# Kernel tuning notes

Measured on AMD Instinct MI355X. Metric: run time of the kernel, lower is better.

Reference implementation:

```python
import jax, jax.numpy as jnp
import numpy as np

EMB = 768
HEADS = 8
HEAD_DIM = EMB // HEADS
SCALE = HEAD_DIM ** -0.5


def setup_inputs() -> dict:
    key = jax.random.key(0)
    ks = jax.random.split(key, 9)
    s = EMB ** -0.5
    return {
        "x": jax.random.normal(ks[0], (2, 4096, EMB), dtype=jnp.float32),
        "Wq": jax.random.normal(ks[1], (EMB, EMB), dtype=jnp.float32) * s,
        "bq": jax.random.normal(ks[2], (EMB,), dtype=jnp.float32) * 0.02,
        "Wk": jax.random.normal(ks[3], (EMB, EMB), dtype=jnp.float32) * s,
        "bk": jax.random.normal(ks[4], (EMB,), dtype=jnp.float32) * 0.02,
        "Wv": jax.random.normal(ks[5], (EMB, EMB), dtype=jnp.float32) * s,
        "bv": jax.random.normal(ks[6], (EMB,), dtype=jnp.float32) * 0.02,
        "Wo": jax.random.normal(ks[7], (EMB, EMB), dtype=jnp.float32) * s,
        "bo": jax.random.normal(ks[8], (EMB,), dtype=jnp.float32) * 0.02,
    }


def reference(x, Wq, bq, Wk, bk, Wv, bv, Wo, bo):
    b, n, _ = x.shape
    def split_heads(t):  # [b, n, emb] -> [b, h, n, d]
        return t.reshape(b, n, HEADS, HEAD_DIM).transpose(0, 2, 1, 3)
    q = split_heads(x @ Wq + bq)
    k = split_heads(x @ Wk + bk)
    v = split_heads(x @ Wv + bv)
    scores = jnp.einsum('bhqd,bhkd->bhqk', q, k)
    # NOTE: faithful to source — softmax first, THEN multiply by scale.
    attn = jax.nn.softmax(scores, axis=-1) * SCALE
    out = jnp.einsum('bhqk,bhkd->bhqd', attn, v)
    out = out.transpose(0, 2, 1, 3).reshape(b, n, EMB)
    return out @ Wo + bo
```

## Files before the change

### kernel.cpp

```cpp
#include <hip/hip_runtime.h>
#include <hip/hip_fp16.h>


typedef _Float16 half8 __attribute__((ext_vector_type(8)));
typedef _Float16 half4 __attribute__((ext_vector_type(4)));
typedef float   float4_ __attribute__((ext_vector_type(4)));
typedef float   f32x16 __attribute__((ext_vector_type(16)));

#define EMB   768
#define NSEQ  4096
#define MTOT  8192
#define SCALE 0.102062072615966f

__device__ __forceinline__ float4_ mfma16(half8 a, half8 b, float4_ c) {
    return __builtin_amdgcn_mfma_f32_16x16x32_f16(a, b, c, 0, 0, 0);
}
__device__ __forceinline__ f32x16 mfma32(half8 a, half8 b, f32x16 c) {
    return __builtin_amdgcn_mfma_f32_32x32x16_f16(a, b, c, 0, 0, 0);
}


__global__ void cast_x(const float* __restrict__ x, _Float16* __restrict__ xb) {
    int i = blockIdx.x * 256 + threadIdx.x;
    float4_ v = ((const float4_*)x)[i];
    half4 h = { (_Float16)v[0], (_Float16)v[1], (_Float16)v[2], (_Float16)v[3] };
    ((half4*)xb)[i] = h;
}

__global__ void prep_w(const float* __restrict__ Wq, const float* __restrict__ Wk,
                       const float* __restrict__ Wv, const float* __restrict__ Wo,
                       _Float16* __restrict__ wqkv, _Float16* __restrict__ wot) {
    int k = blockIdx.x * 256 + threadIdx.x;
    int r = blockIdx.y;
    if (r < 2304) {
        const float* W = (r < 768) ? Wq : (r < 1536) ? Wk : Wv;
        int c = r % 768;
        wqkv[(size_t)r * 768 + k] = (_Float16)W[(size_t)k * 768 + c];
    } else {
        int c = r - 2304;
        wot[(size_t)c * 768 + k] = (_Float16)Wo[(size_t)k * 768 + c];
    }
}

__global__ void prep_bias(const float* __restrict__ bq, const float* __restrict__ bk,
                          const float* __restrict__ bv, float* __restrict__ bqkv) {
    int i = blockIdx.x * 256 + threadIdx.x;
    float v = (i < 768) ? bq[i] : (i < 1536) ? bk[i - 768] : bv[i - 1536];
    bqkv[i] = v;
}

__global__ __launch_bounds__(256, 2) void gemm_kernel(
    const _Float16* __restrict__ A, const _Float16* __restrict__ Bt,
    const float* __restrict__ bias, int mode,
    _Float16* __restrict__ Qo, _Float16* __restrict__ Ko, _Float16* __restrict__ Vto,
    float* __restrict__ out)
{
    __shared__ alignas(16) _Float16 Al[128 * 72];
    __shared__ alignas(16) _Float16 Bl[64 * 72];
    const int tid = threadIdx.x;
    const int lane = tid & 63, w = tid >> 6;
    const int wm = w >> 1, wn = w & 1;
    const int l15 = lane & 15, l4 = lane >> 4;
    const int m0 = blockIdx.y * 128;
    const int n0 = blockIdx.x * 64;

    float4_ acc[4][2] = {};

    for (int k0 = 0; k0 < 768; k0 += 64) {
        #pragma unroll
        for (int it = 0; it < 4; ++it) {
            int idx = it * 256 + tid;
            int row = idx >> 3, c8 = idx & 7;
            *(half8*)(Al + row * 72 + c8 * 8) =
                *(const half8*)(A + (size_t)(m0 + row) * 768 + k0 + c8 * 8);
        }
        #pragma unroll
        for (int it = 0; it < 2; ++it) {
            int idx = it * 256 + tid;
            int row = idx >> 3, c8 = idx & 7;
            *(half8*)(Bl + row * 72 + c8 * 8) =
                *(const half8*)(Bt + (size_t)(n0 + row) * 768 + k0 + c8 * 8);
        }
        __syncthreads();
        #pragma unroll
        for (int kc = 0; kc < 2; ++kc) {
            half8 bfr[2];
            #pragma unroll
            for (int nt = 0; nt < 2; ++nt)
                bfr[nt] = *(const half8*)(Bl + (wn * 32 + nt * 16 + l15) * 72 + kc * 32 + 8 * l4);
            #pragma unroll
            for (int mt = 0; mt < 4; ++mt) {
                half8 afr = *(const half8*)(Al + (wm * 64 + mt * 16 + l15) * 72 + kc * 32 + 8 * l4);
                #pragma unroll
                for (int nt = 0; nt < 2; ++nt)
                    acc[mt][nt] = mfma16(afr, bfr[nt], acc[mt][nt]);
            }
        }
        __syncthreads();
    }

    #pragma unroll
    for (int mt = 0; mt < 4; ++mt)
    #pragma unroll
    for (int nt = 0; nt < 2; ++nt) {
        int gc = n0 + wn * 32 + nt * 16 + l15;
        float bv_ = bias[gc];
        #pragma unroll
        for (int r = 0; r < 4; ++r) {
            int gm = m0 + wm * 64 + mt * 16 + l4 * 4 + r;
            float val = acc[mt][nt][r] + bv_;
            if (mode == 1) {
                out[(size_t)gm * 768 + gc] = val;
            } else {
                int b = gm >> 12, n = gm & 4095;
                _Float16 hv = (_Float16)val;
                if (gc < 768) {
                    int h = gc / 96, d = gc % 96;
                    Qo[(((size_t)(b * 8 + h)) * 4096 + n) * 96 + d] = hv;
                } else if (gc < 1536) {
                    int c = gc - 768, h = c / 96, d = c % 96;
                    int bh = b * 8 + h;
                    size_t idx = (((size_t)bh * 128 + (n >> 5)) * 6 + (d >> 4)) * 512
                               + (size_t)((d >> 3) & 1) * 256 + (size_t)(n & 31) * 8 + (d & 7);
                    Ko[idx] = hv;
                } else {
                    int c = gc - 1536, h = c / 96, d = c % 96;
                    int bh = b * 8 + h;
                    size_t idx = (((size_t)bh * 64 + (n >> 6)) * 12 + ((n >> 4) & 3) * 3 + (d >> 5)) * 512
                               + (size_t)((n >> 3) & 1) * 256 + (size_t)(d & 31) * 8 + (n & 7);
                    Vto[idx] = hv;
                }
            }
        }
    }
}

__global__ __launch_bounds__(256, 2) void attn_kernel(
    const _Float16* __restrict__ Q, const _Float16* __restrict__ Kf,
    const _Float16* __restrict__ Vf, _Float16* __restrict__ AO)
{
    __shared__ alignas(16) _Float16 lds[2][24 * 512];
    __shared__ float tab[4][32];

    const int tid = threadIdx.x;
    const int lane = tid & 63, w = tid >> 6;
    const int l31 = lane & 31, hi = lane >> 5;

    const int B = blockIdx.x;
    const int xcd = B & 7, j = B >> 3;
    const int bh = 2 * xcd + (j >> 5);
    const int qb = j & 31;
    const int q0 = qb * 128 + w * 32;

    const size_t qBase = (size_t)bh * 4096 * 96;
    const _Float16* kfb = Kf + (size_t)bh * 393216;
    const _Float16* vfb = Vf + (size_t)bh * 393216;

    half8 qf[6];
    #pragma unroll
    for (int dch = 0; dch < 6; ++dch)
        qf[dch] = *(const half8*)(Q + qBase + (size_t)(q0 + l31) * 96 + dch * 16 + hi * 8);

    f32x16 o0 = {}, o1 = {}, o2 = {};
    float m_run = -1e30f, l_run = 0.f;

    const int fbase = w * 6;
    half8 streg[6];

    #pragma unroll
    for (int i = 0; i < 6; ++i) {
        int f = fbase + i;
        const _Float16* g = (f < 12 ? kfb + (size_t)f * 512
                                    : vfb + (size_t)(f - 12) * 512) + lane * 8;
        streg[i] = *(const half8*)g;
    }
    #pragma unroll
    for (int i = 0; i < 6; ++i)
        *(half8*)(&lds[0][(fbase + i) * 512 + lane * 8]) = streg[i];
    __syncthreads();

    int cur = 0;
    for (int t = 0; t < 64; ++t) {
        const int tn = (t + 1) & 63;
        #pragma unroll
        for (int i = 0; i < 6; ++i) {
            int f = fbase + i;
            const _Float16* g = (f < 12 ? kfb + ((size_t)tn * 12 + f) * 512
                                        : vfb + ((size_t)tn * 12 + (f - 12)) * 512) + lane * 8;
            streg[i] = *(const half8*)g;
        }

        const _Float16* kb = &lds[cur][0];
        const _Float16* vb = &lds[cur][12 * 512];

        f32x16 s0 = {}, s1 = {};
        __builtin_amdgcn_s_setprio(1);
        #pragma unroll
        for (int dch = 0; dch < 6; ++dch) {
            half8 k0 = *(const half8*)(kb + (0 * 6 + dch) * 512 + lane * 8);
            half8 k1 = *(const half8*)(kb + (1 * 6 + dch) * 512 + lane * 8);
            s0 = mfma32(k0, qf[dch], s0);
            s1 = mfma32(k1, qf[dch], s1);
        }
        __builtin_amdgcn_s_setprio(0);

        float lm = s0[0];
        #pragma unroll
        for (int r = 1; r < 16; ++r) lm = fmaxf(lm, s0[r]);
        #pragma unroll
        for (int r = 0; r < 16; ++r) lm = fmaxf(lm, s1[r]);
        float pmax = fmaxf(lm, __shfl_xor(lm, 32));
        if (__any(pmax > m_run + 4.0f)) {
            float mnew = fmaxf(m_run, pmax);
            float al = __expf(m_run - mnew);
            m_run = mnew;
            l_run *= al;
            if (hi == 0) tab[w][l31] = al;
            asm volatile("s_waitcnt lgkmcnt(0)" ::: "memory");
            #pragma unroll
            for (int r = 0; r < 16; ++r) {
                float alr = tab[w][(r & 3) + 8 * (r >> 2) + 4 * hi];
                o0[r] *= alr; o1[r] *= alr; o2[r] *= alr;
            }
        }
        float ls = 0.f;
        uint32_t Lp0[8], Lp1[8];
        #pragma unroll
        for (int jg = 0; jg < 4; ++jg) {
            float p0 = __expf(s0[4 * jg + 0] - m_run);
            float p1 = __expf(s0[4 * jg + 1] - m_run);
            float p2 = __expf(s0[4 * jg + 2] - m_run);
            float p3 = __expf(s0[4 * jg + 3] - m_run);
            ls += (p0 + p1) + (p2 + p3);
            union { _Float16 h[2]; uint32_t u; } a, b2;
            a.h[0] = (_Float16)p0; a.h[1] = (_Float16)p1;
            b2.h[0] = (_Float16)p2; b2.h[1] = (_Float16)p3;
            Lp0[jg * 2] = a.u; Lp0[jg * 2 + 1] = b2.u;
        }
        #pragma unroll
        for (int jg = 0; jg < 4; ++jg) {
            float p0 = __expf(s1[4 * jg + 0] - m_run);
            float p1 = __expf(s1[4 * jg + 1] - m_run);
            float p2 = __expf(s1[4 * jg + 2] - m_run);
            float p3 = __expf(s1[4 * jg + 3] - m_run);
            ls += (p0 + p1) + (p2 + p3);
            union { _Float16 h[2]; uint32_t u; } a, b2;
            a.h[0] = (_Float16)p0; a.h[1] = (_Float16)p1;
            b2.h[0] = (_Float16)p2; b2.h[1] = (_Float16)p3;
            Lp1[jg * 2] = a.u; Lp1[jg * 2 + 1] = b2.u;
        }
        l_run += ls + __shfl_xor(ls, 32);

        half8 pa[4];
        #pragma unroll
        for (int kc = 0; kc < 2; ++kc) {
            uint32_t a0 = Lp0[4 * kc], a1 = Lp0[4 * kc + 1];
            uint32_t a2 = Lp0[4 * kc + 2], a3 = Lp0[4 * kc + 3];
            uint32_t w0 = __shfl_xor((int)a0, 32), w1 = __shfl_xor((int)a1, 32);
            uint32_t w2 = __shfl_xor((int)a2, 32), w3 = __shfl_xor((int)a3, 32);
            union { half8 h; uint32_t u[4]; } fr;
            fr.u[0] = hi ? w2 : a0;  fr.u[1] = hi ? w3 : a1;
            fr.u[2] = hi ? a2 : w0;  fr.u[3] = hi ? a3 : w1;
            pa[kc] = fr.h;
        }
        #pragma unroll
        for (int kc = 0; kc < 2; ++kc) {
            uint32_t a0 = Lp1[4 * kc], a1 = Lp1[4 * kc + 1];
            uint32_t a2 = Lp1[4 * kc + 2], a3 = Lp1[4 * kc + 3];
            uint32_t w0 = __shfl_xor((int)a0, 32), w1 = __shfl_xor((int)a1, 32);
            uint32_t w2 = __shfl_xor((int)a2, 32), w3 = __shfl_xor((int)a3, 32);
            union { half8 h; uint32_t u[4]; } fr;
            fr.u[0] = hi ? w2 : a0;  fr.u[1] = hi ? w3 : a1;
            fr.u[2] = hi ? a2 : w0;  fr.u[3] = hi ? a3 : w1;
            pa[2 + kc] = fr.h;
        }

        __builtin_amdgcn_s_setprio(1);
        #pragma unroll
        for (int kk = 0; kk < 4; ++kk) {
            half8 v0 = *(const half8*)(vb + (kk * 3 + 0) * 512 + lane * 8);
            half8 v1 = *(const half8*)(vb + (kk * 3 + 1) * 512 + lane * 8);
            half8 v2 = *(const half8*)(vb + (kk * 3 + 2) * 512 + lane * 8);
            o0 = mfma32(pa[kk], v0, o0);
            o1 = mfma32(pa[kk], v1, o1);
            o2 = mfma32(pa[kk], v2, o2);
        }
        __builtin_amdgcn_s_setprio(0);

        __syncthreads();
        #pragma unroll
        for (int i = 0; i < 6; ++i)
            *(half8*)(&lds[cur ^ 1][(fbase + i) * 512 + lane * 8]) = streg[i];
        __syncthreads();
        cur ^= 1;
    }

    if (hi == 0) tab[w][l31] = l_run;
    asm volatile("s_waitcnt lgkmcnt(0)" ::: "memory");
    const int b = bh >> 3, h = bh & 7;
    #pragma unroll
    for (int r = 0; r < 16; ++r) {
        int qrow = (r & 3) + 8 * (r >> 2) + 4 * hi;
        float inv = SCALE / tab[w][qrow];
        int n = q0 + qrow;
        size_t base = ((size_t)(b * 4096 + n)) * 768 + h * 96 + l31;
        AO[base]      = (_Float16)(o0[r] * inv);
        AO[base + 32] = (_Float16)(o1[r] * inv);
        AO[base + 64] = (_Float16)(o2[r] * inv);
    }
}


extern "C" void kernel_launch(void* const* d_in, const int* in_sizes, int n_in,
                              void* d_out, int out_size, void* d_ws, size_t ws_size,
                              hipStream_t stream) {
    const float* x  = (const float*)d_in[0];
    const float* Wq = (const float*)d_in[1];
    const float* bq = (const float*)d_in[2];
    const float* Wk = (const float*)d_in[3];
    const float* bk = (const float*)d_in[4];
    const float* Wv = (const float*)d_in[5];
    const float* bv = (const float*)d_in[6];
    const float* Wo = (const float*)d_in[7];
    const float* bo = (const float*)d_in[8];
    float* out = (float*)d_out;

    char* ws = (char*)d_ws;
    _Float16* xb   = (_Float16*)(ws);
    _Float16* wqkv = (_Float16*)(ws + 12582912);
    _Float16* wot  = (_Float16*)(ws + 16121856);
    float*    bqkv = (float*)   (ws + 17301504);
    _Float16* Qb   = (_Float16*)(ws + 17310720);
    _Float16* Kfb  = (_Float16*)(ws + 29893632);
    _Float16* Vfb  = (_Float16*)(ws + 42476544);
    _Float16* AO   = xb;

    cast_x<<<6144, 256, 0, stream>>>(x, xb);
    prep_w<<<dim3(3, 3072), 256, 0, stream>>>(Wq, Wk, Wv, Wo, wqkv, wot);
    prep_bias<<<9, 256, 0, stream>>>(bq, bk, bv, bqkv);

    gemm_kernel<<<dim3(36, 64), 256, 0, stream>>>(xb, wqkv, bqkv, 0, Qb, Kfb, Vfb, nullptr);

    attn_kernel<<<512, 256, 0, stream>>>(Qb, Kfb, Vfb, AO);

    gemm_kernel<<<dim3(12, 64), 256, 0, stream>>>(AO, wot, bo, 1, nullptr, nullptr, nullptr, out);
}
```

Measured before the change: 281.5 us.

## Tile transpose in prep_w, direct-to-LDS loads, bigger GEMM tiles, two query groups per attention wave

The weight prep now transposes through a shared-memory tile with vectorized, coalesced reads and writes. The GEMM switches to 128x128 tiles loaded straight into LDS with global_load_lds, stored in fragment order. The attention kernel processes 64 query rows per wave as two groups, so each K/V LDS load feeds twice the MFMA work. The attention kernel also fetches the next K/V tile directly into LDS, drops one barrier, folds log2e into Q for exp2, raises the rescale threshold, and uses permlane32_swap instead of shuffles. The cost is higher register pressure (launch bounds of 1) and half as many attention blocks (256 instead of 512), which may underfill the GPU.

```diff
diff --git a/kernel.cpp b/kernel.cpp
--- a/kernel.cpp
+++ b/kernel.cpp
@@ -7,16 +7,19 @@
 typedef float   float4_ __attribute__((ext_vector_type(4)));
 typedef float   f32x16 __attribute__((ext_vector_type(16)));
 
-#define EMB   768
-#define NSEQ  4096
-#define MTOT  8192
 #define SCALE 0.102062072615966f
+#define LOG2E 1.44269504088896340736f
 
 __device__ __forceinline__ float4_ mfma16(half8 a, half8 b, float4_ c) {
     return __builtin_amdgcn_mfma_f32_16x16x32_f16(a, b, c, 0, 0, 0);
 }
 __device__ __forceinline__ f32x16 mfma32(half8 a, half8 b, f32x16 c) {
     return __builtin_amdgcn_mfma_f32_32x32x16_f16(a, b, c, 0, 0, 0);
+}
+__device__ __forceinline__ void gload16(const _Float16* g, _Float16* l) {
+    __builtin_amdgcn_global_load_lds(
+        (const __attribute__((address_space(1))) void*)g,
+        (__attribute__((address_space(3))) void*)l, 16, 0, 0);
 }
 
 
@@ -30,16 +33,34 @@
 __global__ void prep_w(const float* __restrict__ Wq, const float* __restrict__ Wk,
                        const float* __restrict__ Wv, const float* __restrict__ Wo,
                        _Float16* __restrict__ wqkv, _Float16* __restrict__ wot) {
-    int k = blockIdx.x * 256 + threadIdx.x;
-    int r = blockIdx.y;
-    if (r < 2304) {
-        const float* W = (r < 768) ? Wq : (r < 1536) ? Wk : Wv;
-        int c = r % 768;
-        wqkv[(size_t)r * 768 + k] = (_Float16)W[(size_t)k * 768 + c];
-    } else {
-        int c = r - 2304;
-        wot[(size_t)c * 768 + k] = (_Float16)Wo[(size_t)k * 768 + c];
-    }
+    __shared__ float tile[64][65];
+    const int bid = blockIdx.x;
+    const int mat = bid / 144, rem = bid % 144;
+    const int kt = rem / 12, ct = rem % 12;
+    const float* W = (mat == 0) ? Wq : (mat == 1) ? Wk : (mat == 2) ? Wv : Wo;
+    const int k0 = kt * 64, c0 = ct * 64;
+    const int t = threadIdx.x;
+    const int lr = t >> 4, lc = (t & 15) * 4;
+    #pragma unroll
+    for (int i = 0; i < 4; ++i) {
+        float4_ v = *(const float4_*)(W + (size_t)(k0 + i * 16 + lr) * 768 + c0 + lc);
+        tile[i * 16 + lr][lc + 0] = v[0];
+        tile[i * 16 + lr][lc + 1] = v[1];
+        tile[i * 16 + lr][lc + 2] = v[2];
+        tile[i * 16 + lr][lc + 3] = v[3];
+    }
+    __syncthreads();
+    const int cr = t >> 2, kq = (t & 3) * 16;
+    _Float16* dst = (mat < 3) ? (wqkv + ((size_t)(mat * 768 + c0 + cr)) * 768 + k0 + kq)
+                              : (wot  + ((size_t)(c0 + cr)) * 768 + k0 + kq);
+    half8 h0, h1;
+    #pragma unroll
+    for (int j = 0; j < 8; ++j) {
+        h0[j] = (_Float16)tile[kq + j][cr];
+        h1[j] = (_Float16)tile[kq + 8 + j][cr];
+    }
+    *(half8*)dst = h0;
+    *(half8*)(dst + 8) = h1;
 }
 
 __global__ void prep_bias(const float* __restrict__ bq, const float* __restrict__ bk,
@@ -55,44 +76,44 @@
     _Float16* __restrict__ Qo, _Float16* __restrict__ Ko, _Float16* __restrict__ Vto,
     float* __restrict__ out)
 {
-    __shared__ alignas(16) _Float16 Al[128 * 72];
-    __shared__ alignas(16) _Float16 Bl[64 * 72];
+    __shared__ alignas(16) _Float16 Af[16 * 512];
+    __shared__ alignas(16) _Float16 Bf[16 * 512];
     const int tid = threadIdx.x;
     const int lane = tid & 63, w = tid >> 6;
     const int wm = w >> 1, wn = w & 1;
     const int l15 = lane & 15, l4 = lane >> 4;
     const int m0 = blockIdx.y * 128;
-    const int n0 = blockIdx.x * 64;
-
-    float4_ acc[4][2] = {};
+    const int n0 = blockIdx.x * 128;
+
+    const _Float16* gs[8];
+    _Float16* ld[8];
+    #pragma unroll
+    for (int i = 0; i < 8; ++i) {
+        int f = (w & 1) * 8 + i;
+        int rg = f >> 1, kc = f & 1;
+        int r0 = ((w < 2) ? m0 : n0) + rg * 16;
+        gs[i] = ((w < 2) ? A : Bt) + (size_t)(r0 + l15) * 768 + kc * 32 + l4 * 8;
+        ld[i] = ((w < 2) ? Af : Bf) + f * 512;
+    }
+
+    float4_ acc[4][4] = {};
 
     for (int k0 = 0; k0 < 768; k0 += 64) {
         #pragma unroll
-        for (int it = 0; it < 4; ++it) {
-            int idx = it * 256 + tid;
-            int row = idx >> 3, c8 = idx & 7;
-            *(half8*)(Al + row * 72 + c8 * 8) =
-                *(const half8*)(A + (size_t)(m0 + row) * 768 + k0 + c8 * 8);
-        }
-        #pragma unroll
-        for (int it = 0; it < 2; ++it) {
-            int idx = it * 256 + tid;
-            int row = idx >> 3, c8 = idx & 7;
-            *(half8*)(Bl + row * 72 + c8 * 8) =
-                *(const half8*)(Bt + (size_t)(n0 + row) * 768 + k0 + c8 * 8);
-        }
+        for (int i = 0; i < 8; ++i)
+            gload16(gs[i] + k0, ld[i]);
         __syncthreads();
         #pragma unroll
         for (int kc = 0; kc < 2; ++kc) {
-            half8 bfr[2];
+            half8 bfr[4];
             #pragma unroll
-            for (int nt = 0; nt < 2; ++nt)
-                bfr[nt] = *(const half8*)(Bl + (wn * 32 + nt * 16 + l15) * 72 + kc * 32 + 8 * l4);
+            for (int nt = 0; nt < 4; ++nt)
+                bfr[nt] = *(const half8*)(Bf + (size_t)(((wn * 4 + nt) * 2 + kc) * 512 + lane * 8));
             #pragma unroll
             for (int mt = 0; mt < 4; ++mt) {
-                half8 afr = *(const half8*)(Al + (wm * 64 + mt * 16 + l15) * 72 + kc * 32 + 8 * l4);
+                half8 afr = *(const half8*)(Af + (size_t)(((wm * 4 + mt) * 2 + kc) * 512 + lane * 8));
                 #pragma unroll
-                for (int nt = 0; nt < 2; ++nt)
+                for (int nt = 0; nt < 4; ++nt)
                     acc[mt][nt] = mfma16(afr, bfr[nt], acc[mt][nt]);
             }
         }
@@ -102,8 +123,8 @@
     #pragma unroll
     for (int mt = 0; mt < 4; ++mt)
     #pragma unroll
-    for (int nt = 0; nt < 2; ++nt) {
-        int gc = n0 + wn * 32 + nt * 16 + l15;
+    for (int nt = 0; nt < 4; ++nt) {
+        int gc = n0 + wn * 64 + nt * 16 + l15;
         float bv_ = bias[gc];
         #pragma unroll
         for (int r = 0; r < 4; ++r) {
@@ -113,34 +134,33 @@
                 out[(size_t)gm * 768 + gc] = val;
             } else {
                 int b = gm >> 12, n = gm & 4095;
-                _Float16 hv = (_Float16)val;
                 if (gc < 768) {
                     int h = gc / 96, d = gc % 96;
-                    Qo[(((size_t)(b * 8 + h)) * 4096 + n) * 96 + d] = hv;
+                    Qo[(((size_t)(b * 8 + h)) * 4096 + n) * 96 + d] = (_Float16)(val * LOG2E);
                 } else if (gc < 1536) {
                     int c = gc - 768, h = c / 96, d = c % 96;
                     int bh = b * 8 + h;
                     size_t idx = (((size_t)bh * 128 + (n >> 5)) * 6 + (d >> 4)) * 512
                                + (size_t)((d >> 3) & 1) * 256 + (size_t)(n & 31) * 8 + (d & 7);
-                    Ko[idx] = hv;
+                    Ko[idx] = (_Float16)val;
                 } else {
                     int c = gc - 1536, h = c / 96, d = c % 96;
                     int bh = b * 8 + h;
                     size_t idx = (((size_t)bh * 64 + (n >> 6)) * 12 + ((n >> 4) & 3) * 3 + (d >> 5)) * 512
                                + (size_t)((n >> 3) & 1) * 256 + (size_t)(d & 31) * 8 + (n & 7);
-                    Vto[idx] = hv;
+                    Vto[idx] = (_Float16)val;
                 }
             }
         }
     }
 }
 
-__global__ __launch_bounds__(256, 2) void attn_kernel(
+__global__ __launch_bounds__(256, 1) void attn_kernel(
     const _Float16* __restrict__ Q, const _Float16* __restrict__ Kf,
     const _Float16* __restrict__ Vf, _Float16* __restrict__ AO)
 {
-    __shared__ alignas(16) _Float16 lds[2][24 * 512];
-    __shared__ float tab[4][32];
+    __shared__ alignas(16) _Float16 kvbuf[2][24 * 512];
+    __shared__ float tab[4][64];
 
     const int tid = threadIdx.x;
     const int lane = tid & 63, w = tid >> 6;
@@ -148,132 +168,114 @@
 
     const int B = blockIdx.x;
     const int xcd = B & 7, j = B >> 3;
-    const int bh = 2 * xcd + (j >> 5);
-    const int qb = j & 31;
-    const int q0 = qb * 128 + w * 32;
+    const int bh = 2 * xcd + (j >> 4);
+    const int qb = j & 15;
+    const int q0 = qb * 256 + w * 64;
 
     const size_t qBase = (size_t)bh * 4096 * 96;
     const _Float16* kfb = Kf + (size_t)bh * 393216;
     const _Float16* vfb = Vf + (size_t)bh * 393216;
 
-    half8 qf[6];
-    #pragma unroll
-    for (int dch = 0; dch < 6; ++dch)
-        qf[dch] = *(const half8*)(Q + qBase + (size_t)(q0 + l31) * 96 + dch * 16 + hi * 8);
-
-    f32x16 o0 = {}, o1 = {}, o2 = {};
-    float m_run = -1e30f, l_run = 0.f;
+    half8 qf[2][6];
+    #pragma unroll
+    for (int g = 0; g < 2; ++g)
+        #pragma unroll
+        for (int dch = 0; dch < 6; ++dch)
+            qf[g][dch] = *(const half8*)(Q + qBase + (size_t)(q0 + g * 32 + l31) * 96 + dch * 16 + hi * 8);
+
+    f32x16 oA0 = {}, oA1 = {}, oA2 = {}, oB0 = {}, oB1 = {}, oB2 = {};
+    float mA = -1e30f, lA = 0.f, mB = -1e30f, lB = 0.f;
 
     const int fbase = w * 6;
-    half8 streg[6];
-
+    const _Float16* gsrc[6];
     #pragma unroll
     for (int i = 0; i < 6; ++i) {
         int f = fbase + i;
-        const _Float16* g = (f < 12 ? kfb + (size_t)f * 512
-                                    : vfb + (size_t)(f - 12) * 512) + lane * 8;
-        streg[i] = *(const half8*)g;
-    }
+        gsrc[i] = ((f < 12) ? (kfb + (size_t)f * 512) : (vfb + (size_t)(f - 12) * 512)) + lane * 8;
+    }
+
     #pragma unroll
     for (int i = 0; i < 6; ++i)
-        *(half8*)(&lds[0][(fbase + i) * 512 + lane * 8]) = streg[i];
+        gload16(gsrc[i], &kvbuf[0][(fbase + i) * 512]);
     __syncthreads();
+
+    auto softmax_group = [&](f32x16& s0, f32x16& s1, float& m, float& l,
+                             f32x16& o0, f32x16& o1, f32x16& o2, int trow, half8* pa) {
+        float lm = fmaxf(s0[0], s0[1]);
+        #pragma unroll
+        for (int r = 2; r < 16; ++r) lm = fmaxf(lm, s0[r]);
+        #pragma unroll
+        for (int r = 0; r < 16; ++r) lm = fmaxf(lm, s1[r]);
+        float pmax = fmaxf(lm, __shfl_xor(lm, 32));
+        if (__any(pmax > m + 8.0f)) {
+            float mn = fmaxf(m, pmax);
+            float al = __builtin_exp2f(m - mn);
+            m = mn; l *= al;
+            if (hi == 0) tab[w][trow + l31] = al;
+            asm volatile("s_waitcnt lgkmcnt(0)" ::: "memory");
+            #pragma unroll
+            for (int r = 0; r < 16; ++r) {
+                float alr = tab[w][trow + (r & 3) + 8 * (r >> 2) + 4 * hi];
+                o0[r] *= alr; o1[r] *= alr; o2[r] *= alr;
+            }
+        }
+        float ls = 0.f;
+        uint32_t Lp[16];
+        #pragma unroll
+        for (int kg = 0; kg < 2; ++kg) {
+            const f32x16& s = kg ? s1 : s0;
+            #pragma unroll
+            for (int jg = 0; jg < 4; ++jg) {
+                float p0 = __builtin_exp2f(s[4 * jg + 0] - m);
+                float p1 = __builtin_exp2f(s[4 * jg + 1] - m);
+                float p2 = __builtin_exp2f(s[4 * jg + 2] - m);
+                float p3 = __builtin_exp2f(s[4 * jg + 3] - m);
+                ls += (p0 + p1) + (p2 + p3);
+                union { _Float16 h[2]; uint32_t u; } pk0, pk1;
+                pk0.h[0] = (_Float16)p0; pk0.h[1] = (_Float16)p1;
+                pk1.h[0] = (_Float16)p2; pk1.h[1] = (_Float16)p3;
+                Lp[kg * 8 + jg * 2] = pk0.u; Lp[kg * 8 + jg * 2 + 1] = pk1.u;
+            }
+        }
+        l += ls + __shfl_xor(ls, 32);
+        #pragma unroll
+        for (int kk = 0; kk < 4; ++kk) {
+            uint32_t u0 = Lp[4 * kk], u1 = Lp[4 * kk + 1];
+            uint32_t u2 = Lp[4 * kk + 2], u3 = Lp[4 * kk + 3];
+            asm("v_permlane32_swap_b32 %0, %1" : "+v"(u0), "+v"(u2));
+            asm("v_permlane32_swap_b32 %0, %1" : "+v"(u1), "+v"(u3));
+            union { half8 h; uint32_t u[4]; } fr;
+            fr.u[0] = u0; fr.u[1] = u1; fr.u[2] = u2; fr.u[3] = u3;
+            pa[kk] = fr.h;
+        }
+    };
 
     int cur = 0;
     for (int t = 0; t < 64; ++t) {
         const int tn = (t + 1) & 63;
         #pragma unroll
-        for (int i = 0; i < 6; ++i) {
-            int f = fbase + i;
-            const _Float16* g = (f < 12 ? kfb + ((size_t)tn * 12 + f) * 512
-                                        : vfb + ((size_t)tn * 12 + (f - 12)) * 512) + lane * 8;
-            streg[i] = *(const half8*)g;
-        }
-
-        const _Float16* kb = &lds[cur][0];
-        const _Float16* vb = &lds[cur][12 * 512];
-
-        f32x16 s0 = {}, s1 = {};
+        for (int i = 0; i < 6; ++i)
+            gload16(gsrc[i] + (size_t)tn * 6144, &kvbuf[cur ^ 1][(fbase + i) * 512]);
+
+        const _Float16* kb = &kvbuf[cur][0];
+        const _Float16* vb = &kvbuf[cur][12 * 512];
+
+        f32x16 sA0 = {}, sA1 = {}, sB0 = {}, sB1 = {};
         __builtin_amdgcn_s_setprio(1);
         #pragma unroll
         for (int dch = 0; dch < 6; ++dch) {
-            half8 k0 = *(const half8*)(kb + (0 * 6 + dch) * 512 + lane * 8);
-            half8 k1 = *(const half8*)(kb + (1 * 6 + dch) * 512 + lane * 8);
-            s0 = mfma32(k0, qf[dch], s0);
-            s1 = mfma32(k1, qf[dch], s1);
+            half8 k0 = *(const half8*)(kb + (dch) * 512 + lane * 8);
+            half8 k1 = *(const half8*)(kb + (6 + dch) * 512 + lane * 8);
+            sA0 = mfma32(k0, qf[0][dch], sA0);
+            sB0 = mfma32(k0, qf[1][dch], sB0);
+            sA1 = mfma32(k1, qf[0][dch], sA1);
+            sB1 = mfma32(k1, qf[1][dch], sB1);
         }
         __builtin_amdgcn_s_setprio(0);
 
-        float lm = s0[0];
-        #pragma unroll
-        for (int r = 1; r < 16; ++r) lm = fmaxf(lm, s0[r]);
-        #pragma unroll
-        for (int r = 0; r < 16; ++r) lm = fmaxf(lm, s1[r]);
-        float pmax = fmaxf(lm, __shfl_xor(lm, 32));
-        if (__any(pmax > m_run + 4.0f)) {
-            float mnew = fmaxf(m_run, pmax);
-            float al = __expf(m_run - mnew);
-            m_run = mnew;
-            l_run *= al;
-            if (hi == 0) tab[w][l31] = al;
-            asm volatile("s_waitcnt lgkmcnt(0)" ::: "memory");
-            #pragma unroll
-            for (int r = 0; r < 16; ++r) {
-                float alr = tab[w][(r & 3) + 8 * (r >> 2) + 4 * hi];
-                o0[r] *= alr; o1[r] *= alr; o2[r] *= alr;
-            }
-        }
-        float ls = 0.f;
-        uint32_t Lp0[8], Lp1[8];
-        #pragma unroll
-        for (int jg = 0; jg < 4; ++jg) {
-            float p0 = __expf(s0[4 * jg + 0] - m_run);
-            float p1 = __expf(s0[4 * jg + 1] - m_run);
-            float p2 = __expf(s0[4 * jg + 2] - m_run);
-            float p3 = __expf(s0[4 * jg + 3] - m_run);
-            ls += (p0 + p1) + (p2 + p3);
-            union { _Float16 h[2]; uint32_t u; } a, b2;
-            a.h[0] = (_Float16)p0; a.h[1] = (_Float16)p1;
-            b2.h[0] = (_Float16)p2; b2.h[1] = (_Float16)p3;
-            Lp0[jg * 2] = a.u; Lp0[jg * 2 + 1] = b2.u;
-        }
-        #pragma unroll
-        for (int jg = 0; jg < 4; ++jg) {
-            float p0 = __expf(s1[4 * jg + 0] - m_run);
-            float p1 = __expf(s1[4 * jg + 1] - m_run);
-            float p2 = __expf(s1[4 * jg + 2] - m_run);
-            float p3 = __expf(s1[4 * jg + 3] - m_run);
-            ls += (p0 + p1) + (p2 + p3);
-            union { _Float16 h[2]; uint32_t u; } a, b2;
-            a.h[0] = (_Float16)p0; a.h[1] = (_Float16)p1;
-            b2.h[0] = (_Float16)p2; b2.h[1] = (_Float16)p3;
-            Lp1[jg * 2] = a.u; Lp1[jg * 2 + 1] = b2.u;
-        }
-        l_run += ls + __shfl_xor(ls, 32);
-
-        half8 pa[4];
-        #pragma unroll
-        for (int kc = 0; kc < 2; ++kc) {
-            uint32_t a0 = Lp0[4 * kc], a1 = Lp0[4 * kc + 1];
-            uint32_t a2 = Lp0[4 * kc + 2], a3 = Lp0[4 * kc + 3];
-            uint32_t w0 = __shfl_xor((int)a0, 32), w1 = __shfl_xor((int)a1, 32);
-            uint32_t w2 = __shfl_xor((int)a2, 32), w3 = __shfl_xor((int)a3, 32);
-            union { half8 h; uint32_t u[4]; } fr;
-            fr.u[0] = hi ? w2 : a0;  fr.u[1] = hi ? w3 : a1;
-            fr.u[2] = hi ? a2 : w0;  fr.u[3] = hi ? a3 : w1;
-            pa[kc] = fr.h;
-        }
-        #pragma unroll
-        for (int kc = 0; kc < 2; ++kc) {
-            uint32_t a0 = Lp1[4 * kc], a1 = Lp1[4 * kc + 1];
-            uint32_t a2 = Lp1[4 * kc + 2], a3 = Lp1[4 * kc + 3];
-            uint32_t w0 = __shfl_xor((int)a0, 32), w1 = __shfl_xor((int)a1, 32);
-            uint32_t w2 = __shfl_xor((int)a2, 32), w3 = __shfl_xor((int)a3, 32);
-            union { half8 h; uint32_t u[4]; } fr;
-            fr.u[0] = hi ? w2 : a0;  fr.u[1] = hi ? w3 : a1;
-            fr.u[2] = hi ? a2 : w0;  fr.u[3] = hi ? a3 : w1;
-            pa[2 + kc] = fr.h;
-        }
+        half8 paA[4], paB[4];
+        softmax_group(sA0, sA1, mA, lA, oA0, oA1, oA2, 0, paA);
+        softmax_group(sB0, sB1, mB, lB, oB0, oB1, oB2, 32, paB);
 
         __builtin_amdgcn_s_setprio(1);
         #pragma unroll
@@ -281,32 +283,36 @@
             half8 v0 = *(const half8*)(vb + (kk * 3 + 0) * 512 + lane * 8);
             half8 v1 = *(const half8*)(vb + (kk * 3 + 1) * 512 + lane * 8);
             half8 v2 = *(const half8*)(vb + (kk * 3 + 2) * 512 + lane * 8);
-            o0 = mfma32(pa[kk], v0, o0);
-            o1 = mfma32(pa[kk], v1, o1);
-            o2 = mfma32(pa[kk], v2, o2);
+            oA0 = mfma32(paA[kk], v0, oA0);
+            oB0 = mfma32(paB[kk], v0, oB0);
+            oA1 = mfma32(paA[kk], v1, oA1);
+            oB1 = mfma32(paB[kk], v1, oB1);
+            oA2 = mfma32(paA[kk], v2, oA2);
+            oB2 = mfma32(paB[kk], v2, oB2);
         }
         __builtin_amdgcn_s_setprio(0);
 
-        __syncthreads();
-        #pragma unroll
-        for (int i = 0; i < 6; ++i)
-            *(half8*)(&lds[cur ^ 1][(fbase + i) * 512 + lane * 8]) = streg[i];
         __syncthreads();
         cur ^= 1;
     }
 
-    if (hi == 0) tab[w][l31] = l_run;
+    if (hi == 0) { tab[w][l31] = lA; tab[w][32 + l31] = lB; }
     asm volatile("s_waitcnt lgkmcnt(0)" ::: "memory");
     const int b = bh >> 3, h = bh & 7;
     #pragma unroll
     for (int r = 0; r < 16; ++r) {
         int qrow = (r & 3) + 8 * (r >> 2) + 4 * hi;
-        float inv = SCALE / tab[w][qrow];
-        int n = q0 + qrow;
-        size_t base = ((size_t)(b * 4096 + n)) * 768 + h * 96 + l31;
-        AO[base]      = (_Float16)(o0[r] * inv);
-        AO[base + 32] = (_Float16)(o1[r] * inv);
-        AO[base + 64] = (_Float16)(o2[r] * inv);
+        float invA = SCALE / tab[w][qrow];
+        float invB = SCALE / tab[w][32 + qrow];
+        int nA = q0 + qrow, nB = q0 + 32 + qrow;
+        size_t baseA = ((size_t)(b * 4096 + nA)) * 768 + h * 96 + l31;
+        size_t baseB = ((size_t)(b * 4096 + nB)) * 768 + h * 96 + l31;
+        AO[baseA]      = (_Float16)(oA0[r] * invA);
+        AO[baseA + 32] = (_Float16)(oA1[r] * invA);
+        AO[baseA + 64] = (_Float16)(oA2[r] * invA);
+        AO[baseB]      = (_Float16)(oB0[r] * invB);
+        AO[baseB + 32] = (_Float16)(oB1[r] * invB);
+        AO[baseB + 64] = (_Float16)(oB2[r] * invB);
     }
 }
 
@@ -336,12 +342,12 @@
     _Float16* AO   = xb;
 
     cast_x<<<6144, 256, 0, stream>>>(x, xb);
-    prep_w<<<dim3(3, 3072), 256, 0, stream>>>(Wq, Wk, Wv, Wo, wqkv, wot);
+    prep_w<<<576, 256, 0, stream>>>(Wq, Wk, Wv, Wo, wqkv, wot);
     prep_bias<<<9, 256, 0, stream>>>(bq, bk, bv, bqkv);
 
-    gemm_kernel<<<dim3(36, 64), 256, 0, stream>>>(xb, wqkv, bqkv, 0, Qb, Kfb, Vfb, nullptr);
-
-    attn_kernel<<<512, 256, 0, stream>>>(Qb, Kfb, Vfb, AO);
-
-    gemm_kernel<<<dim3(12, 64), 256, 0, stream>>>(AO, wot, bo, 1, nullptr, nullptr, nullptr, out);
-}
+    gemm_kernel<<<dim3(18, 64), 256, 0, stream>>>(xb, wqkv, bqkv, 0, Qb, Kfb, Vfb, nullptr);
+
+    attn_kernel<<<256, 256, 0, stream>>>(Qb, Kfb, Vfb, AO);
+
+    gemm_kernel<<<dim3(6, 64), 256, 0, stream>>>(AO, wot, bo, 1, nullptr, nullptr, nullptr, out);
+}
```

After: 315.2 us. 1.12x slower.
